# Kernel tuning notes

Hardware: AMD Instinct MI355X
Metric: run time of the kernel (lower is better)

The kernel has to match this reference:

```python
import jax, jax.numpy as jnp
import numpy as np

B, L, LS, H, E, F, V = 32, 64, 100, 512, 512, 64, 32000
SOS = 2
EPS = 1e-6


def setup_inputs() -> dict:
    key = jax.random.key(0)
    ks = jax.random.split(key, 16)
    s = 0.05
    inp = dict(
        h0=jax.random.normal(ks[0], (B, H), jnp.float32),
        c0=jax.random.normal(ks[1], (B, H), jnp.float32),
        input_embeddings=jax.random.normal(ks[2], (B, L, E), jnp.float32),
        encoder_output=jax.random.normal(ks[3], (B, LS, H), jnp.float32),
        field_embedding=jax.random.normal(ks[4], (B, LS, F), jnp.float32),
        embedding=jax.random.normal(ks[5], (V, E), jnp.float32) * s,
        lstm_W=jax.random.normal(ks[6], (E + H, 4 * H), jnp.float32) * s,
        lstm_b=jnp.zeros((4 * H,), jnp.float32),
        Wh=jax.random.normal(ks[7], (H, H), jnp.float32) * s,
        bh=jnp.zeros((H,), jnp.float32),
        Ws=jax.random.normal(ks[8], (H, H), jnp.float32) * s,
        bs=jnp.zeros((H,), jnp.float32),
        Wr=jax.random.normal(ks[9], (H, H), jnp.float32) * s,
        br=jnp.zeros((H,), jnp.float32),
        Wf=jax.random.normal(ks[10], (F, H), jnp.float32) * s,
        bf=jnp.zeros((H,), jnp.float32),
        Wo=jax.random.normal(ks[11], (2 * H, H), jnp.float32) * s,
        bo=jnp.zeros((H,), jnp.float32),
        out_W=jax.random.normal(ks[12], (H, V), jnp.float32) * s,
        out_b=jnp.zeros((V,), jnp.float32),
    )
    lens = jax.random.randint(ks[13], (B,), L // 2, L + 1)
    # pin max length to L so the data-dependent while-loop becomes a static scan
    inp["inputs_len"] = lens.at[0].set(L)
    return inp


def _masked_softmax(scores):  # [B, LS], matches exp/(1e-6+sum) normalization
    w = jnp.exp(scores - jnp.max(scores, axis=1, keepdims=True))
    return w / (EPS + jnp.sum(w, axis=1, keepdims=True))


def reference(h0, c0, input_embeddings, encoder_output, field_embedding,
              embedding, lstm_W, lstm_b, Wh, bh, Ws, bs, Wr, br, Wf, bf,
              Wo, bo, out_W, out_b, inputs_len):
    # precompute attention keys (set_attention_hiddenstate)
    phi_hs = jnp.tanh(encoder_output @ Wh + bh)    # [B, LS, H]
    phi_fds = jnp.tanh(field_embedding @ Wf + bf)  # [B, LS, H]

    def step(carry, xs):
        h_prev, c_prev = carry
        x, finished = xs                 # [B,E], [B] bool
        mask = finished[:, None]
        # LstmUnit
        z = jnp.concatenate([x, h_prev], -1) @ lstm_W + lstm_b
        i, j, f, o = jnp.split(z, 4, axis=-1)
        c = jax.nn.sigmoid(f + 1.0) * c_prev + jax.nn.sigmoid(i) * jnp.tanh(j)
        h = jax.nn.sigmoid(o) * jnp.tanh(c)
        o_t = jnp.where(mask, 0.0, h)
        h_new = jnp.where(mask, h_prev, h)
        c_new = jnp.where(mask, c_prev, c)
        # FieldDualAttentionWrapper
        gamma = jnp.tanh(o_t @ Ws + bs)  # [B,H]
        alpha = jnp.tanh(o_t @ Wr + br)  # [B,H]
        w_h = _masked_softmax(jnp.einsum('blh,bh->bl', phi_hs, gamma))
        w_f = _masked_softmax(jnp.einsum('blh,bh->bl', phi_fds, alpha))
        w = w_h * w_f
        w = w / (EPS + jnp.sum(w, axis=1, keepdims=True))
        context = jnp.einsum('bl,blh->bh', w, encoder_output)
        att = jnp.tanh(jnp.concatenate([context, o_t], -1) @ Wo + bo)
        att = jnp.where(mask, 0.0, att)
        # OutputUnit
        logits = att @ out_W + out_b
        logits = jnp.where(mask, 0.0, logits)
        return (h_new, c_new), logits

    b = h0.shape[0]
    x0 = jnp.broadcast_to(embedding[SOS], (b, embedding.shape[1]))
    finished0 = jnp.zeros((b,), bool)
    carry, logits0 = step((h0, c0), (x0, finished0))

    xs = jnp.swapaxes(input_embeddings, 0, 1)                       # [L,B,E]
    fin = jnp.arange(xs.shape[0])[:, None] >= inputs_len[None, :]   # [L,B]
    carry, logits_seq = jax.lax.scan(step, carry, (xs, fin))

    emit = jnp.concatenate([logits0[None], logits_seq], 0)  # [L+1,B,V]
    emit = jnp.swapaxes(emit, 0, 1)                          # [B,L+1,V]
    return emit, carry[0], carry[1]
```

## Files before the change

kernel.cpp:

```cpp
#include <hip/hip_runtime.h>
#include <math.h>

#define B_ 32
#define L_ 64
#define T_ 65
#define LS_ 100
#define H_ 512
#define E_ 512
#define F_ 64
#define V_ 32000
#define SOS_ 2
#define EPS_ 1e-6f

typedef __attribute__((ext_vector_type(8))) _Float16 half8;
typedef __attribute__((ext_vector_type(4))) float f32x4;

__device__ __forceinline__ float sigmoidf_(float x) { return 1.0f / (1.0f + expf(-x)); }

__device__ __forceinline__ void gload_lds16(const void* g, void* l) {
    __builtin_amdgcn_global_load_lds(
        (const __attribute__((address_space(1))) unsigned int*)g,
        (__attribute__((address_space(3))) unsigned int*)l, 16, 0, 0);
}

__global__ void build_X(const float* __restrict__ emb,
                        const float* __restrict__ inp_emb,
                        _Float16* __restrict__ X) {
    int idx = blockIdx.x * blockDim.x + threadIdx.x;
    if (idx >= T_ * B_ * E_) return;
    int e = idx % E_;
    int r = idx / E_;
    int t = r / B_, b = r % B_;
    float v;
    if (t == 0) v = emb[(size_t)SOS_ * E_ + e];
    else        v = inp_emb[((size_t)b * L_ + (t - 1)) * E_ + e];
    X[idx] = (_Float16)v;
}

__global__ void init_state(const float* __restrict__ h0, const float* __restrict__ c0,
                           float* __restrict__ h_all, float* __restrict__ c_all) {
    int idx = blockIdx.x * blockDim.x + threadIdx.x;
    if (idx < B_ * H_) { h_all[idx] = h0[idx]; c_all[idx] = c0[idx]; }
}

__global__ void convert_f16(const float* __restrict__ src, _Float16* __restrict__ dst, int n) {
    int idx = blockIdx.x * blockDim.x + threadIdx.x;
    if (idx < n) dst[idx] = (_Float16)src[idx];
}

__global__ void build_bsr(const float* __restrict__ bs, const float* __restrict__ br,
                          float* __restrict__ bsr) {
    int idx = blockIdx.x * blockDim.x + threadIdx.x;
    if (idx < H_) { bsr[idx] = bs[idx]; bsr[H_ + idx] = br[idx]; }
}

__global__ void transpose_f32(const float* __restrict__ src, float* __restrict__ dst,
                              int R, int C) {
    __shared__ float tl[32][33];
    int r0 = blockIdx.y * 32, c0 = blockIdx.x * 32;
    int cx = threadIdx.x & 31, g = threadIdx.x >> 5;
#pragma unroll
    for (int i = 0; i < 4; i++) {
        int ry = g * 4 + i;
        tl[ry][cx] = src[(size_t)(r0 + ry) * C + c0 + cx];
    }
    __syncthreads();
#pragma unroll
    for (int i = 0; i < 4; i++) {
        int cy = g * 4 + i;
        dst[(size_t)(c0 + cy) * R + r0 + cx] = tl[cx][cy];
    }
}

__global__ void transpose_f32_to_f16(const float* __restrict__ src,
                                     _Float16* __restrict__ dst, int R, int C) {
    __shared__ float tl[32][33];
    int r0 = blockIdx.y * 32, c0 = blockIdx.x * 32;
    int cx = threadIdx.x & 31, g = threadIdx.x >> 5;
#pragma unroll
    for (int i = 0; i < 4; i++) {
        int ry = g * 4 + i;
        tl[ry][cx] = src[(size_t)(r0 + ry) * C + c0 + cx];
    }
    __syncthreads();
#pragma unroll
    for (int i = 0; i < 4; i++) {
        int cy = g * 4 + i;
        dst[(size_t)(c0 + cy) * R + r0 + cx] = (_Float16)tl[cx][cy];
    }
}

template <bool TANH, bool MASK, bool OUTF16, bool EMIT>
__global__ __launch_bounds__(256) void gemm_mfma(
        const _Float16* __restrict__ A, int lda,
        const _Float16* __restrict__ Bt,
        const float* __restrict__ bias, void* __restrict__ Cout,
        int M, int N, int K, const int* __restrict__ lens) {
    __shared__ __align__(16) _Float16 As[128 * 32];
    __shared__ __align__(16) _Float16 Bs[128 * 32];

    int bm = blockIdx.y * 128;
    int bn = blockIdx.x * 128;
    int tid = threadIdx.x;
    int wave = tid >> 6, lane = tid & 63;

    int wm = (wave & 1) * 64;
    int wn = (wave >> 1) * 64;

    f32x4 acc[4][4];
#pragma unroll
    for (int i = 0; i < 4; i++)
#pragma unroll
        for (int j = 0; j < 4; j++) acc[i][j] = (f32x4){0.f, 0.f, 0.f, 0.f};

    int srow = wave * 16 + (lane >> 2);
    int skoff = (lane & 3) * 8;

    for (int k0 = 0; k0 < K; k0 += 32) {
#pragma unroll
        for (int p = 0; p < 2; p++) {
            int r = p * 64 + srow;
            int ar = bm + r; if (ar > M - 1) ar = M - 1;
            gload_lds16(A + (size_t)ar * lda + k0 + skoff,
                        (void*)(As + (size_t)(p * 64 + wave * 16) * 32));
            gload_lds16(Bt + (size_t)(bn + r) * K + k0 + skoff,
                        (void*)(Bs + (size_t)(p * 64 + wave * 16) * 32));
        }
        __syncthreads();

        int mrow = wm + (lane & 15);
        int nrow = wn + (lane & 15);
        int kq = (lane >> 4) * 8;
        half8 afr[4], bfr[4];
#pragma unroll
        for (int i = 0; i < 4; i++)
            afr[i] = *(const half8*)&As[(mrow + i * 16) * 32 + kq];
#pragma unroll
        for (int j = 0; j < 4; j++)
            bfr[j] = *(const half8*)&Bs[(nrow + j * 16) * 32 + kq];
#pragma unroll
        for (int i = 0; i < 4; i++)
#pragma unroll
            for (int j = 0; j < 4; j++)
                acc[i][j] = __builtin_amdgcn_mfma_f32_16x16x32_f16(
                    afr[i], bfr[j], acc[i][j], 0, 0, 0);
        __syncthreads();
    }

    int lcol = lane & 15, lquad = lane >> 4;
#pragma unroll
    for (int i = 0; i < 4; i++) {
#pragma unroll
        for (int r = 0; r < 4; r++) {
            int gr = bm + wm + i * 16 + lquad * 4 + r;
            if (gr >= M) continue;
            bool fin = false;
            int t = gr >> 5, bb = gr & 31;
            if (MASK) fin = (t > 0) && ((t - 1) >= lens[bb]);
#pragma unroll
            for (int j = 0; j < 4; j++) {
                int gc = bn + wn + j * 16 + lcol;
                float v = acc[i][j][r] + bias[gc];
                if (TANH) v = tanhf(v);
                if (MASK && fin) v = 0.f;
                if (EMIT) {
                    ((float*)Cout)[((size_t)bb * T_ + t) * (size_t)V_ + gc] = v;
                } else if (OUTF16) {
                    ((_Float16*)Cout)[(size_t)gr * N + gc] = (_Float16)v;
                } else {
                    ((float*)Cout)[(size_t)gr * N + gc] = v;
                }
            }
        }
    }
}

__global__ __launch_bounds__(256) void lstm_step2(
        const float* __restrict__ Zx, const float* __restrict__ Wht,
        const int* __restrict__ lens,
        float* __restrict__ h_all, float* __restrict__ c_all,
        _Float16* __restrict__ ao_concat, int t) {
    __shared__ float Wl[16 * 516];
    __shared__ float zb[32 * 20];

    int tid = threadIdx.x;
    int j0 = blockIdx.x * 4;
    const float* h_prev = h_all + (size_t)t * B_ * H_;

    {
        int c = tid >> 4, s = tid & 15;
        int col = (c >> 2) * H_ + j0 + (c & 3);
        const float* src = Wht + (size_t)col * H_ + s * 32;
        float* dstp = Wl + c * 516 + s * 32;
#pragma unroll
        for (int i = 0; i < 8; i++)
            *(f32x4*)(dstp + i * 4) = *(const f32x4*)(src + i * 4);
    }
    __syncthreads();

    int bt = tid >> 6;
    int ct = (tid >> 4) & 3;
    int s  = tid & 15;

    float acc[8][4];
#pragma unroll
    for (int bi = 0; bi < 8; bi++)
#pragma unroll
        for (int cc = 0; cc < 4; cc++) acc[bi][cc] = 0.f;

#pragma unroll
    for (int q = 0; q < 8; q++) {
        int kbase = q * 64 + s * 4;
        f32x4 w4[4];
#pragma unroll
        for (int cc = 0; cc < 4; cc++)
            w4[cc] = *(const f32x4*)&Wl[(ct * 4 + cc) * 516 + kbase];
        f32x4 h4[8];
#pragma unroll
        for (int bi = 0; bi < 8; bi++)
            h4[bi] = *(const f32x4*)&h_prev[(size_t)(bt * 8 + bi) * H_ + kbase];
#pragma unroll
        for (int bi = 0; bi < 8; bi++)
#pragma unroll
            for (int cc = 0; cc < 4; cc++)
                acc[bi][cc] += h4[bi].x * w4[cc].x + h4[bi].y * w4[cc].y +
                               h4[bi].z * w4[cc].z + h4[bi].w * w4[cc].w;
    }

#pragma unroll
    for (int off = 8; off >= 1; off >>= 1)
#pragma unroll
        for (int bi = 0; bi < 8; bi++)
#pragma unroll
            for (int cc = 0; cc < 4; cc++)
                acc[bi][cc] += __shfl_down(acc[bi][cc], off);

    if (s == 0) {
#pragma unroll
        for (int bi = 0; bi < 8; bi++) {
            int b = bt * 8 + bi;
            f32x4 zx = *(const f32x4*)&Zx[((size_t)t * B_ + b) * (4 * H_) + ct * H_ + j0];
            f32x4 v;
            v.x = acc[bi][0] + zx.x; v.y = acc[bi][1] + zx.y;
            v.z = acc[bi][2] + zx.z; v.w = acc[bi][3] + zx.w;
            *(f32x4*)&zb[b * 20 + ct * 4] = v;
        }
    }
    __syncthreads();

    if (tid < 128) {
        int b = tid >> 2, cj = tid & 3;
        int j = j0 + cj;
        float zi = zb[b * 20 + 0 + cj];
        float zj = zb[b * 20 + 4 + cj];
        float zf = zb[b * 20 + 8 + cj];
        float zo = zb[b * 20 + 12 + cj];
        float cp = c_all[(size_t)t * B_ * H_ + (size_t)b * H_ + j];
        float hp = h_prev[(size_t)b * H_ + j];
        float c = sigmoidf_(zf + 1.0f) * cp + sigmoidf_(zi) * tanhf(zj);
        float h = sigmoidf_(zo) * tanhf(c);
        bool fin = (t > 0) && ((t - 1) >= lens[b]);
        h_all[(size_t)(t + 1) * B_ * H_ + (size_t)b * H_ + j] = fin ? hp : h;
        c_all[(size_t)(t + 1) * B_ * H_ + (size_t)b * H_ + j] = fin ? cp : c;
        ao_concat[((size_t)t * B_ + b) * 1024 + 512 + j] = (_Float16)(fin ? 0.f : h);
    }
}

__global__ __launch_bounds__(256) void attention_kernel(
        const _Float16* __restrict__ phi_hs,
        const _Float16* __restrict__ phi_fds,
        const float* __restrict__ ga,
        const float* __restrict__ enc,
        _Float16* __restrict__ ao_concat) {
    int r = blockIdx.x;
    int b = r % B_;
    int tid = threadIdx.x;
    int wave = tid >> 6, lane = tid & 63;

    __shared__ float sh[LS_], sf[LS_];
    __shared__ float red[8];

    const float* gw = ga + (size_t)r * 1024;
    f32x4 g0 = *(const f32x4*)&gw[lane * 8];
    f32x4 g1 = *(const f32x4*)&gw[lane * 8 + 4];
    f32x4 a0 = *(const f32x4*)&gw[512 + lane * 8];
    f32x4 a1 = *(const f32x4*)&gw[512 + lane * 8 + 4];

    const _Float16* phb = phi_hs + (size_t)b * LS_ * H_ + lane * 8;
    const _Float16* pfb = phi_fds + (size_t)b * LS_ * H_ + lane * 8;

    for (int l = wave; l < LS_; l += 4) {
        half8 ph = *(const half8*)(phb + (size_t)l * H_);
        half8 pf = *(const half8*)(pfb + (size_t)l * H_);
        float s1 = (float)ph[0] * g0.x + (float)ph[1] * g0.y +
                   (float)ph[2] * g0.z + (float)ph[3] * g0.w +
                   (float)ph[4] * g1.x + (float)ph[5] * g1.y +
                   (float)ph[6] * g1.z + (float)ph[7] * g1.w;
        float s2 = (float)pf[0] * a0.x + (float)pf[1] * a0.y +
                   (float)pf[2] * a0.z + (float)pf[3] * a0.w +
                   (float)pf[4] * a1.x + (float)pf[5] * a1.y +
                   (float)pf[6] * a1.z + (float)pf[7] * a1.w;
#pragma unroll
        for (int off = 32; off; off >>= 1) {
            s1 += __shfl_xor(s1, off);
            s2 += __shfl_xor(s2, off);
        }
        if (lane == 0) { sh[l] = s1; sf[l] = s2; }
    }
    __syncthreads();

    float v1 = (tid < LS_) ? sh[tid] : -1e30f;
    float v2 = (tid < LS_) ? sf[tid] : -1e30f;
    float m1 = v1, m2 = v2;
#pragma unroll
    for (int off = 32; off; off >>= 1) {
        m1 = fmaxf(m1, __shfl_xor(m1, off));
        m2 = fmaxf(m2, __shfl_xor(m2, off));
    }
    if (tid < 128 && lane == 0) { red[wave * 2] = m1; red[wave * 2 + 1] = m2; }
    __syncthreads();
    m1 = fmaxf(red[0], red[2]);
    m2 = fmaxf(red[1], red[3]);

    float e1 = (tid < LS_) ? expf(v1 - m1) : 0.f;
    float e2 = (tid < LS_) ? expf(v2 - m2) : 0.f;
    float s1 = e1, s2 = e2;
#pragma unroll
    for (int off = 32; off; off >>= 1) {
        s1 += __shfl_xor(s1, off);
        s2 += __shfl_xor(s2, off);
    }
    if (tid < 128 && lane == 0) { red[4 + wave * 2] = s1; red[4 + wave * 2 + 1] = s2; }
    __syncthreads();
    float r1 = 1.f / (EPS_ + red[4] + red[6]);
    float r2 = 1.f / (EPS_ + red[5] + red[7]);

    float w = (e1 * r1) * (e2 * r2);
    float s3 = w;
#pragma unroll
    for (int off = 32; off; off >>= 1) s3 += __shfl_xor(s3, off);
    __syncthreads();
    if (tid < 128 && lane == 0) red[wave] = s3;
    __syncthreads();
    float r3 = 1.f / (EPS_ + red[0] + red[1]);
    if (tid < LS_) sh[tid] = w * r3;
    __syncthreads();

    const float* eb = enc + (size_t)b * LS_ * H_;
    float acc0 = 0.f, acc1 = 0.f;
#pragma unroll 4
    for (int l = 0; l < LS_; l++) {
        float wl = sh[l];
        acc0 += wl * eb[(size_t)l * H_ + tid];
        acc1 += wl * eb[(size_t)l * H_ + tid + 256];
    }
    ao_concat[(size_t)r * 1024 + tid] = (_Float16)acc0;
    ao_concat[(size_t)r * 1024 + tid + 256] = (_Float16)acc1;
}

__global__ void write_final(const float* __restrict__ h_all, const float* __restrict__ c_all,
                            float* __restrict__ out) {
    int idx = blockIdx.x * blockDim.x + threadIdx.x;
    if (idx < B_ * H_) {
        size_t base = (size_t)B_ * T_ * V_;
        out[base + idx] = h_all[(size_t)T_ * B_ * H_ + idx];
        out[base + B_ * H_ + idx] = c_all[(size_t)T_ * B_ * H_ + idx];
    }
}

extern "C" void kernel_launch(void* const* d_in, const int* in_sizes, int n_in,
                              void* d_out, int out_size, void* d_ws, size_t ws_size,
                              hipStream_t stream) {
    const float* h0   = (const float*)d_in[0];
    const float* c0   = (const float*)d_in[1];
    const float* inp_emb = (const float*)d_in[2];
    const float* enc  = (const float*)d_in[3];
    const float* fld  = (const float*)d_in[4];
    const float* emb  = (const float*)d_in[5];
    const float* lstm_W = (const float*)d_in[6];
    const float* lstm_b = (const float*)d_in[7];
    const float* Wh = (const float*)d_in[8];
    const float* bh = (const float*)d_in[9];
    const float* Ws = (const float*)d_in[10];
    const float* bs = (const float*)d_in[11];
    const float* Wr = (const float*)d_in[12];
    const float* br = (const float*)d_in[13];
    const float* Wf = (const float*)d_in[14];
    const float* bfp = (const float*)d_in[15];
    const float* Wo = (const float*)d_in[16];
    const float* bo = (const float*)d_in[17];
    const float* out_W = (const float*)d_in[18];
    const float* out_b = (const float*)d_in[19];
    const int*   lens  = (const int*)d_in[20];
    float* out = (float*)d_out;

    char* p = (char*)d_ws;
    auto alloc = [&](size_t bytes) { char* r = p; p += (bytes + 255) & ~(size_t)255; return r; };

    char* region = p;
    float*    Zx    = (float*)   alloc((size_t)T_ * B_ * 4 * H_ * 4);
    float*    ga    = (float*)   alloc((size_t)T_ * B_ * 1024 * 4);
    _Float16* X_h   = (_Float16*)alloc((size_t)T_ * B_ * E_ * 2);
    _Float16* enc_h = (_Float16*)alloc((size_t)B_ * LS_ * H_ * 2);
    _Float16* Wxt_h = (_Float16*)alloc((size_t)4 * H_ * E_ * 2);
    _Float16* Wt_h  = (_Float16*)region;
    _Float16* phi_hs_h  = (_Float16*)alloc((size_t)B_ * LS_ * H_ * 2);
    _Float16* phi_fds_h = (_Float16*)alloc((size_t)B_ * LS_ * H_ * 2);
    float*    h_all = (float*)alloc((size_t)(T_ + 1) * B_ * H_ * 4);
    float*    c_all = (float*)alloc((size_t)(T_ + 1) * B_ * H_ * 4);
    _Float16* ao_h  = (_Float16*)alloc((size_t)T_ * B_ * 1024 * 2);
    float*    Wht   = (float*)alloc((size_t)4 * H_ * H_ * 4);
    _Float16* fld_h = (_Float16*)alloc((size_t)B_ * LS_ * F_ * 2);
    _Float16* Wh_t  = (_Float16*)alloc((size_t)H_ * H_ * 2);
    _Float16* Wsr_t = (_Float16*)alloc((size_t)1024 * H_ * 2);
    _Float16* Wo_t  = (_Float16*)alloc((size_t)H_ * 1024 * 2);
    _Float16* Wf_t  = (_Float16*)alloc((size_t)H_ * F_ * 2);
    _Float16* att_h = (_Float16*)alloc((size_t)T_ * B_ * H_ * 2);
    float*    bsr   = (float*)alloc(1024 * 4);

    build_X<<<(T_ * B_ * E_ + 255) / 256, 256, 0, stream>>>(emb, inp_emb, X_h);
    init_state<<<(B_ * H_ + 255) / 256, 256, 0, stream>>>(h0, c0, h_all, c_all);
    build_bsr<<<2, 256, 0, stream>>>(bs, br, bsr);
    convert_f16<<<(B_ * LS_ * H_ + 255) / 256, 256, 0, stream>>>(enc, enc_h, B_ * LS_ * H_);
    convert_f16<<<(B_ * LS_ * F_ + 255) / 256, 256, 0, stream>>>(fld, fld_h, B_ * LS_ * F_);
    {
        dim3 g(4 * H_ / 32, H_ / 32);
        transpose_f32<<<g, 256, 0, stream>>>(lstm_W + (size_t)E_ * 4 * H_, Wht, H_, 4 * H_);
        transpose_f32_to_f16<<<g, 256, 0, stream>>>(lstm_W, Wxt_h, E_, 4 * H_);
    }
    {   dim3 g(H_ / 32, H_ / 32);
        transpose_f32_to_f16<<<g, 256, 0, stream>>>(Wh, Wh_t, H_, H_);
        transpose_f32_to_f16<<<g, 256, 0, stream>>>(Ws, Wsr_t, H_, H_);
        transpose_f32_to_f16<<<g, 256, 0, stream>>>(Wr, Wsr_t + (size_t)H_ * H_, H_, H_);
    }
    {   dim3 g(H_ / 32, F_ / 32);
        transpose_f32_to_f16<<<g, 256, 0, stream>>>(Wf, Wf_t, F_, H_);
    }
    {   dim3 g(H_ / 32, 1024 / 32);
        transpose_f32_to_f16<<<g, 256, 0, stream>>>(Wo, Wo_t, 1024, H_);
    }

    {   dim3 g(2048 / 128, (T_ * B_ + 127) / 128);
        gemm_mfma<false, false, false, false><<<g, 256, 0, stream>>>(
            X_h, E_, Wxt_h, lstm_b, Zx, T_ * B_, 2048, 512, nullptr);
    }
    {   dim3 g(512 / 128, 3200 / 128);
        gemm_mfma<true, false, true, false><<<g, 256, 0, stream>>>(
            enc_h, H_, Wh_t, bh, phi_hs_h, B_ * LS_, 512, 512, nullptr);
        gemm_mfma<true, false, true, false><<<g, 256, 0, stream>>>(
            fld_h, F_, Wf_t, bfp, phi_fds_h, B_ * LS_, 512, 64, nullptr);
    }
    for (int t = 0; t < T_; t++) {
        lstm_step2<<<128, 256, 0, stream>>>(Zx, Wht, lens, h_all, c_all, ao_h, t);
    }
    {   dim3 g(1024 / 128, (T_ * B_ + 127) / 128);
        gemm_mfma<true, false, false, false><<<g, 256, 0, stream>>>(
            ao_h + 512, 1024, Wsr_t, bsr, ga, T_ * B_, 1024, 512, nullptr);
    }
    attention_kernel<<<T_ * B_, 256, 0, stream>>>(phi_hs_h, phi_fds_h, ga, enc, ao_h);
    {   dim3 g(V_ / 32, 512 / 32);
        transpose_f32_to_f16<<<g, 256, 0, stream>>>(out_W, Wt_h, 512, V_);
    }
    {   dim3 g(512 / 128, (T_ * B_ + 127) / 128);
        gemm_mfma<true, true, true, false><<<g, 256, 0, stream>>>(
            ao_h, 1024, Wo_t, bo, att_h, T_ * B_, 512, 1024, lens);
    }
    {   dim3 g(V_ / 128, (T_ * B_ + 127) / 128);
        gemm_mfma<false, true, false, true><<<g, 256, 0, stream>>>(
            att_h, H_, Wt_h, out_b, out, T_ * B_, V_, 512, lens);
    }
    write_final<<<(B_ * H_ + 255) / 256, 256, 0, stream>>>(h_all, c_all, out);
}
```

Measured before the change: 1.316 ms.

## Fuse per-step LSTM launches into one persistent cooperative kernel with grid sync

Replaces the 65 per-timestep lstm_step2 launches with a single cooperative kernel that loads its slice of the recurrent weights into LDS once, keeps c and previous h in registers, and synchronises all blocks with grid.sync between timesteps. The aim is to remove per-step launch overhead and repeated weight reloads from the sequential recurrence. It depends on cooperative launch support, falls back to the old loop if that launch fails, and grid-wide barriers carry their own cost.

```diff
diff --git a/kernel.cpp b/kernel.cpp
--- a/kernel.cpp
+++ b/kernel.cpp
@@ -1,5 +1,8 @@
 #include <hip/hip_runtime.h>
+#include <hip/hip_cooperative_groups.h>
 #include <math.h>
+
+namespace cg = cooperative_groups;
 
 #define B_ 32
 #define L_ 64
@@ -173,6 +176,113 @@
             }
         }
     }
+}
+
+__global__ __launch_bounds__(256) void lstm_chain(
+        const float* __restrict__ Zx, const float* __restrict__ Wht,
+        const int* __restrict__ lens,
+        float* __restrict__ h_all, float* __restrict__ c_all,
+        _Float16* __restrict__ ao_concat) {
+    cg::grid_group grid = cg::this_grid();
+    __shared__ float Wl[16 * 516];
+    __shared__ float zb[32 * 20];
+
+    int tid = threadIdx.x;
+    int j0 = blockIdx.x * 4;
+
+    {
+        int c = tid >> 4, s = tid & 15;
+        int col = (c >> 2) * H_ + j0 + (c & 3);
+        const float* src = Wht + (size_t)col * H_ + s * 32;
+        float* dstp = Wl + c * 516 + s * 32;
+#pragma unroll
+        for (int i = 0; i < 8; i++)
+            *(f32x4*)(dstp + i * 4) = *(const f32x4*)(src + i * 4);
+    }
+
+    int bt = tid >> 6;
+    int ct = (tid >> 4) & 3;
+    int s  = tid & 15;
+
+    int bq = tid >> 2, cj = tid & 3;
+    float cp = 0.f, hpreg = 0.f;
+    int lenb = 0;
+    if (tid < 128) {
+        cp    = c_all[(size_t)bq * H_ + j0 + cj];
+        hpreg = h_all[(size_t)bq * H_ + j0 + cj];
+        lenb  = lens[bq];
+    }
+    __syncthreads();
+
+    for (int t = 0; t < T_; t++) {
+        const float* h_prev = h_all + (size_t)t * B_ * H_;
+
+        float acc[8][4];
+#pragma unroll
+        for (int bi = 0; bi < 8; bi++)
+#pragma unroll
+            for (int cc = 0; cc < 4; cc++) acc[bi][cc] = 0.f;
+
+#pragma unroll
+        for (int q = 0; q < 8; q++) {
+            int kbase = q * 64 + s * 4;
+            f32x4 w4[4];
+#pragma unroll
+            for (int cc = 0; cc < 4; cc++)
+                w4[cc] = *(const f32x4*)&Wl[(ct * 4 + cc) * 516 + kbase];
+            f32x4 h4[8];
+#pragma unroll
+            for (int bi = 0; bi < 8; bi++)
+                h4[bi] = *(const f32x4*)&h_prev[(size_t)(bt * 8 + bi) * H_ + kbase];
+#pragma unroll
+            for (int bi = 0; bi < 8; bi++)
+#pragma unroll
+                for (int cc = 0; cc < 4; cc++)
+                    acc[bi][cc] += h4[bi].x * w4[cc].x + h4[bi].y * w4[cc].y +
+                                   h4[bi].z * w4[cc].z + h4[bi].w * w4[cc].w;
+        }
+
+#pragma unroll
+        for (int off = 8; off >= 1; off >>= 1)
+#pragma unroll
+            for (int bi = 0; bi < 8; bi++)
+#pragma unroll
+                for (int cc = 0; cc < 4; cc++)
+                    acc[bi][cc] += __shfl_down(acc[bi][cc], off);
+
+        if (s == 0) {
+#pragma unroll
+            for (int bi = 0; bi < 8; bi++) {
+                int b = bt * 8 + bi;
+                f32x4 zx = *(const f32x4*)&Zx[((size_t)t * B_ + b) * (4 * H_) + ct * H_ + j0];
+                f32x4 v;
+                v.x = acc[bi][0] + zx.x; v.y = acc[bi][1] + zx.y;
+                v.z = acc[bi][2] + zx.z; v.w = acc[bi][3] + zx.w;
+                *(f32x4*)&zb[b * 20 + ct * 4] = v;
+            }
+        }
+        __syncthreads();
+
+        if (tid < 128) {
+            float zi = zb[bq * 20 + 0 + cj];
+            float zj = zb[bq * 20 + 4 + cj];
+            float zf = zb[bq * 20 + 8 + cj];
+            float zo = zb[bq * 20 + 12 + cj];
+            float c = sigmoidf_(zf + 1.0f) * cp + sigmoidf_(zi) * tanhf(zj);
+            float h = sigmoidf_(zo) * tanhf(c);
+            bool fin = (t > 0) && ((t - 1) >= lenb);
+            float hn = fin ? hpreg : h;
+            cp = fin ? cp : c;
+            h_all[(size_t)(t + 1) * B_ * H_ + (size_t)bq * H_ + j0 + cj] = hn;
+            ao_concat[((size_t)t * B_ + bq) * 1024 + 512 + (j0 + cj)] =
+                (_Float16)(fin ? 0.f : h);
+            hpreg = hn;
+        }
+        grid.sync();
+    }
+
+    if (tid < 128)
+        c_all[(size_t)T_ * B_ * H_ + (size_t)bq * H_ + j0 + cj] = cp;
 }
 
 __global__ __launch_bounds__(256) void lstm_step2(
@@ -450,8 +560,15 @@
         gemm_mfma<true, false, true, false><<<g, 256, 0, stream>>>(
             fld_h, F_, Wf_t, bfp, phi_fds_h, B_ * LS_, 512, 64, nullptr);
     }
-    for (int t = 0; t < T_; t++) {
-        lstm_step2<<<128, 256, 0, stream>>>(Zx, Wht, lens, h_all, c_all, ao_h, t);
+    {
+        void* args[] = {(void*)&Zx, (void*)&Wht, (void*)&lens,
+                        (void*)&h_all, (void*)&c_all, (void*)&ao_h};
+        hipError_t err = hipLaunchCooperativeKernel(
+            (const void*)lstm_chain, dim3(128), dim3(256), args, 0, stream);
+        if (err != hipSuccess) {
+            for (int t = 0; t < T_; t++)
+                lstm_step2<<<128, 256, 0, stream>>>(Zx, Wht, lens, h_all, c_all, ao_h, t);
+        }
     }
     {   dim3 g(1024 / 128, (T_ * B_ + 127) / 128);
         gemm_mfma<true, false, false, false><<<g, 256, 0, stream>>>(
```

After: 2.255 ms. 1.71x slower.
